# Kernel tuning notes

Measured on AMD Instinct MI355X. Metric: run time of the kernel, lower is better.

The kernel has to match this reference:

```python
import jax, jax.numpy as jnp
import numpy as np

B, Wd, C, H, F = 48, 88, 256, 32, 1024
NH_SELF, NH_CROSS = 8, 8


def _ln(x, g, b, eps=1e-5):
    mu = x.mean(-1, keepdims=True)
    var = ((x - mu) ** 2).mean(-1, keepdims=True)
    return (x - mu) / jnp.sqrt(var + eps) * g + b


def setup_inputs() -> dict:
    key = jax.random.key(0)
    ks = jax.random.split(key, 16)
    s = 0.02  # weight init scale
    d = {
        'pooled_features': jax.random.normal(ks[0], (B, Wd, C), jnp.float32),
        'features': jax.random.normal(ks[1], (B, C, H, Wd), jnp.float32),
        'self_pe': jax.random.normal(ks[2], (Wd, C), jnp.float32),
        'cross_pe': jax.random.normal(ks[3], (H, C), jnp.float32),
    }
    # LayerNorm params
    for n in ['ln_qs', 'ln_vs', 'ln_qc', 'ln_kv', 'ln_vc', 'ln_ffn']:
        d[n + '_g'] = jnp.ones((C,), jnp.float32)
        d[n + '_b'] = jnp.zeros((C,), jnp.float32)
    # attention projections (stored [in,out]; y = x @ W + b)
    names = ['Wq_s', 'Wk_s', 'Wv_s', 'Wp_s', 'Wq_c', 'Wk_c', 'Wv_c', 'Wp_c']
    for i, n in enumerate(names):
        d[n] = jax.random.normal(ks[4 + i], (C, C), jnp.float32) * s
    for n in ['bq_s', 'bv_s', 'bp_s', 'bq_c', 'bv_c', 'bp_c']:
        d[n] = jnp.zeros((C,), jnp.float32)
    # FFN
    d['W1'] = jax.random.normal(ks[12], (C, F), jnp.float32) * s
    d['b1'] = jnp.zeros((F,), jnp.float32)
    d['W2'] = jax.random.normal(ks[13], (F, C), jnp.float32) * s
    d['b2'] = jnp.zeros((C,), jnp.float32)
    return d


def reference(pooled_features, features, self_pe, cross_pe,
              ln_qs_g, ln_qs_b, ln_vs_g, ln_vs_b,
              ln_qc_g, ln_qc_b, ln_kv_g, ln_kv_b, ln_vc_g, ln_vc_b,
              ln_ffn_g, ln_ffn_b,
              Wq_s, bq_s, Wk_s, Wv_s, bv_s, Wp_s, bp_s,
              Wq_c, bq_c, Wk_c, Wv_c, bv_c, Wp_c, bp_c,
              W1, b1, W2, b2):
    b, w, c = pooled_features.shape
    h = features.shape[2]
    ds = c // NH_SELF
    dc = c // NH_CROSS

    # ---- cross attention first (op_order='cross_first', with_pe=True) ----
    xq = pooled_features                                  # [B,W,C]
    qn = _ln(xq, ln_qc_g, ln_qc_b)
    kv = jnp.transpose(features, (0, 3, 2, 1))            # [B,W,H,C]
    kn = _ln(kv + cross_pe[None, None], ln_kv_g, ln_kv_b)
    vn = _ln(kv, ln_vc_g, ln_vc_b)
    q = (qn @ Wq_c + bq_c).reshape(b, w, NH_CROSS, dc)    # query len 1 per column
    k = (kn @ Wk_c).reshape(b, w, h, NH_CROSS, dc)
    v = (vn @ Wv_c + bv_c).reshape(b, w, h, NH_CROSS, dc)
    attn = jnp.einsum('bwhd,bwkhd->bwhk', q, k) * (dc ** -0.5)
    attn = jax.nn.softmax(attn, axis=-1)
    out = jnp.einsum('bwhk,bwkhd->bwhd', attn, v).reshape(b, w, c)
    x = out @ Wp_c + bp_c + xq

    # ---- self attention over width tokens ----
    qn = _ln(x + self_pe[None], ln_qs_g, ln_qs_b)
    vn = _ln(x, ln_vs_g, ln_vs_b)
    q = (qn @ Wq_s + bq_s).reshape(b, w, NH_SELF, ds)
    k = (qn @ Wk_s).reshape(b, w, NH_SELF, ds)
    v = (vn @ Wv_s + bv_s).reshape(b, w, NH_SELF, ds)
    attn = jnp.einsum('bnhd,bmhd->bhnm', q, k) * (ds ** -0.5)
    attn = jax.nn.softmax(attn, axis=-1)
    out = jnp.einsum('bhnm,bmhd->bnhd', attn, v).reshape(b, w, c)
    x = out @ Wp_s + bp_s + x

    # ---- FFN (mmcv FFN, num_fcs=2, GELU, identity residual) ----
    hdn = _ln(x, ln_ffn_g, ln_ffn_b)
    hdn = jax.nn.gelu(hdn @ W1 + b1, approximate=False) @ W2 + b2
    return x + hdn
```

## Files before the change

### kernel.cpp

```cpp
#include <hip/hip_runtime.h>
#include <math.h>

#define B_   48
#define W_   88
#define C_   256
#define H_   32
#define F_   1024
#define BW_  (B_ * W_)
#define BWH_ (B_ * W_ * H_)
#define HW_  (H_ * W_)

typedef float  f32x4  __attribute__((ext_vector_type(4)));
typedef __bf16 bf16x8 __attribute__((ext_vector_type(8)));

__device__ __forceinline__ unsigned short f2bf(float f) {
  union { float f; unsigned int u; } v; v.f = f;
  unsigned int r = v.u + 0x7FFFu + ((v.u >> 16) & 1u);
  return (unsigned short)(r >> 16);
}
__device__ __forceinline__ float bf2f(unsigned short h) {
  union { unsigned int u; float f; } v; v.u = ((unsigned int)h) << 16;
  return v.f;
}

__global__ __launch_bounds__(256) void wt_kernel(const float* __restrict__ src,
                                                 unsigned short* __restrict__ dst,
                                                 int in_dim, int out_dim) {
  int idx = blockIdx.x * 256 + threadIdx.x;
  if (idx >= in_dim * out_dim) return;
  int i = idx % in_dim;
  int o = idx / in_dim;
  dst[idx] = f2bf(src[(size_t)i * out_dim + o]);
}

__global__ __launch_bounds__(256) void mqk_build(
    const float* __restrict__ Wq, const float* __restrict__ Wk,
    const float* __restrict__ bq,
    unsigned short* __restrict__ Mqk, float* __restrict__ bqk) {
  int n = blockIdx.x;
  int h = n >> 8, c = n & 255;
  int t = threadIdx.x;
  __shared__ float wk_s[32];
  if (t < 32) wk_s[t] = Wk[c * 256 + 32 * h + t];
  __syncthreads();
  const float scale = 0.17677669529663689f;
  float acc = 0.f;
#pragma unroll
  for (int dd = 0; dd < 32; dd++) acc += Wq[t * 256 + 32 * h + dd] * wk_s[dd];
  Mqk[(size_t)n * 256 + t] = f2bf(acc * scale);
  if (t == 0) {
    float bb = 0.f;
    for (int dd = 0; dd < 32; dd++) bb += bq[32 * h + dd] * wk_s[dd];
    bqk[n] = bb * scale;
  }
}

__global__ __launch_bounds__(256) void mvp_build(
    const float* __restrict__ Wv, const float* __restrict__ Wp,
    unsigned short* __restrict__ Mvp) {
  int d = blockIdx.x;
  int t = threadIdx.x;
  for (int h = 0; h < 8; h++) {
    float acc = 0.f;
#pragma unroll
    for (int dd = 0; dd < 32; dd++)
      acc += Wv[t * 256 + 32 * h + dd] * Wp[(32 * h + dd) * 256 + d];
    Mvp[(size_t)d * 2048 + h * 256 + t] = f2bf(acc);
  }
}

__global__ void bvp_build(const float* __restrict__ bv, const float* __restrict__ Wp,
                          const float* __restrict__ bp, float* __restrict__ bvp) {
  int d = threadIdx.x;
  float acc = bp[d];
  for (int dp = 0; dp < 256; dp++) acc += bv[dp] * Wp[dp * 256 + d];
  bvp[d] = acc;
}

__global__ __launch_bounds__(256) void ln_transpose2(
    const float* __restrict__ features, const float* __restrict__ cross_pe,
    const float* __restrict__ g_kv, const float* __restrict__ b_kv,
    const float* __restrict__ g_vc, const float* __restrict__ b_vc,
    unsigned short* __restrict__ kn, unsigned short* __restrict__ vn) {
  int b   = blockIdx.x / 88;
  int tl  = blockIdx.x % 88;
  int hw0 = tl * 32;
  __shared__ float tile[32][257];
  __shared__ float st[32][4];
  int tid = threadIdx.x;
  int l4 = (tid & 7) * 4;
  int cc = tid >> 3;
  const float* fb = features + (size_t)b * C_ * HW_ + hw0;
#pragma unroll
  for (int p = 0; p < 8; p++) {
    int c = cc + p * 32;
    float4 v = *(const float4*)(fb + (size_t)c * HW_ + l4);
    tile[l4 + 0][c] = v.x; tile[l4 + 1][c] = v.y;
    tile[l4 + 2][c] = v.z; tile[l4 + 3][c] = v.w;
  }
  __syncthreads();
  int row = tid >> 3, ln = tid & 7;
  int hr = (hw0 + row) / 88;
  const float* per = cross_pe + hr * 256;
  float s1 = 0, s2 = 0, p1 = 0, p2 = 0;
  for (int c = ln; c < 256; c += 8) {
    float v  = tile[row][c];
    float vp = v + per[c];
    s1 += v;  s2 += v * v;
    p1 += vp; p2 += vp * vp;
  }
#pragma unroll
  for (int m = 1; m < 8; m <<= 1) {
    s1 += __shfl_xor(s1, m, 8); s2 += __shfl_xor(s2, m, 8);
    p1 += __shfl_xor(p1, m, 8); p2 += __shfl_xor(p2, m, 8);
  }
  if (ln == 0) {
    float mu  = s1 * (1.f / 256.f);
    float rs  = rsqrtf(s2 * (1.f / 256.f) - mu * mu + 1e-5f);
    float muk = p1 * (1.f / 256.f);
    float rsk = rsqrtf(p2 * (1.f / 256.f) - muk * muk + 1e-5f);
    st[row][0] = mu; st[row][1] = rs; st[row][2] = muk; st[row][3] = rsk;
  }
  __syncthreads();
  int c = tid;
  float gv = g_vc[c], bv2 = b_vc[c], gk = g_kv[c], bk = b_kv[c];
  for (int r = 0; r < 32; r++) {
    int hh = (hw0 + r) / 88, ww = (hw0 + r) % 88;
    float v  = tile[r][c];
    float vp = v + cross_pe[hh * 256 + c];
    size_t ro = ((size_t)b * 88 + ww) * 32 + hh;
    vn[ro * 256 + c] = f2bf((v  - st[r][0]) * st[r][1] * gv + bv2);
    kn[ro * 256 + c] = f2bf((vp - st[r][2]) * st[r][3] * gk + bk);
  }
}

__global__ __launch_bounds__(256) void ln_rows(
    const float* __restrict__ x, const float* __restrict__ pe, int pe_mod,
    const float* __restrict__ g, const float* __restrict__ bta,
    unsigned short* __restrict__ out) {
  int row = blockIdx.x, c = threadIdx.x;
  float v = x[(size_t)row * C_ + c];
  if (pe) v += pe[(size_t)(row % pe_mod) * C_ + c];
  float s1 = v, s2 = v * v;
#pragma unroll
  for (int m = 32; m > 0; m >>= 1) {
    s1 += __shfl_xor(s1, m, 64);
    s2 += __shfl_xor(s2, m, 64);
  }
  __shared__ float red[8];
  int wave = c >> 6;
  if ((c & 63) == 0) { red[wave] = s1; red[4 + wave] = s2; }
  __syncthreads();
  s1 = red[0] + red[1] + red[2] + red[3];
  s2 = red[4] + red[5] + red[6] + red[7];
  float mu = s1 * (1.f / C_);
  float rs = rsqrtf(s2 * (1.f / C_) - mu * mu + 1e-5f);
  out[(size_t)row * C_ + c] = f2bf((v - mu) * rs * g[c] + bta[c]);
}

__global__ __launch_bounds__(256) void gemm_bt(
    const unsigned short* __restrict__ A, const unsigned short* __restrict__ Bt,
    int M, int N, int K,
    const float* __restrict__ bias, const float* __restrict__ resid,
    float* __restrict__ outF, unsigned short* __restrict__ outB, int act_gelu) {
  __shared__ __attribute__((aligned(16))) unsigned short As[64][32];
  __shared__ __attribute__((aligned(16))) unsigned short Bs[64][32];
  const int tiles_n = N >> 6;
  const int bm = blockIdx.x / tiles_n;
  const int bn = blockIdx.x % tiles_n;
  const int tid = threadIdx.x;
  const int wave = tid >> 6, lane = tid & 63;
  const int quad = lane >> 4, lr = lane & 15;
  const int wm = (wave >> 1) << 5, wn = (wave & 1) << 5;
  const int lrow = tid >> 2;
  const int lcol = (tid & 3) << 3;
  const size_t a_base = (size_t)(bm * 64 + lrow) * K + lcol;
  const size_t b_base = (size_t)(bn * 64 + lrow) * K + lcol;
  f32x4 acc[2][2] = {};
  for (int k0 = 0; k0 < K; k0 += 32) {
    *(uint4*)&As[lrow][lcol] = *(const uint4*)(A + a_base + k0);
    *(uint4*)&Bs[lrow][lcol] = *(const uint4*)(Bt + b_base + k0);
    __syncthreads();
    bf16x8 af0 = *(const bf16x8*)&As[wm + lr][quad << 3];
    bf16x8 af1 = *(const bf16x8*)&As[wm + 16 + lr][quad << 3];
    bf16x8 bf0 = *(const bf16x8*)&Bs[wn + lr][quad << 3];
    bf16x8 bf1 = *(const bf16x8*)&Bs[wn + 16 + lr][quad << 3];
    acc[0][0] = __builtin_amdgcn_mfma_f32_16x16x32_bf16(af0, bf0, acc[0][0], 0, 0, 0);
    acc[0][1] = __builtin_amdgcn_mfma_f32_16x16x32_bf16(af0, bf1, acc[0][1], 0, 0, 0);
    acc[1][0] = __builtin_amdgcn_mfma_f32_16x16x32_bf16(af1, bf0, acc[1][0], 0, 0, 0);
    acc[1][1] = __builtin_amdgcn_mfma_f32_16x16x32_bf16(af1, bf1, acc[1][1], 0, 0, 0);
    __syncthreads();
  }
#pragma unroll
  for (int i = 0; i < 2; i++)
#pragma unroll
    for (int j = 0; j < 2; j++)
#pragma unroll
      for (int rr = 0; rr < 4; rr++) {
        int row = bm * 64 + wm + i * 16 + quad * 4 + rr;
        int col = bn * 64 + wn + j * 16 + lr;
        float val = acc[i][j][rr];
        if (bias) val += bias[col];
        if (act_gelu) val = 0.5f * val * (1.f + erff(val * 0.70710678118654752f));
        if (resid) val += resid[(size_t)row * N + col];
        if (outF) outF[(size_t)row * N + col] = val;
        else outB[(size_t)row * N + col] = f2bf(val);
      }
}

#define KSTR 264
__global__ __launch_bounds__(256) void cross_attn2(
    const unsigned short* __restrict__ qt_g,
    const unsigned short* __restrict__ kn, const unsigned short* __restrict__ vn,
    unsigned short* __restrict__ ctx_g) {
  int bw = blockIdx.x;
  int tid = threadIdx.x;
  __shared__ __attribute__((aligned(16))) unsigned short qtl[8][KSTR];
  __shared__ __attribute__((aligned(16))) unsigned short knl[32][KSTR];
  __shared__ __attribute__((aligned(16))) unsigned short vnl[32][KSTR];
  __shared__ float s_sc[32 * 9];
  __shared__ float ps[8 * 36];
  __shared__ __attribute__((aligned(16))) unsigned short ctxl[2048];

  {
    uint4 qv = *(const uint4*)(qt_g + (size_t)bw * 2048 + tid * 8);
    int h = tid >> 5, c0 = (tid & 31) * 8;
    *(uint4*)&qtl[h][c0] = qv;
    int j = tid >> 3, cs = (tid & 7) * 32;
    const unsigned short* kr = kn + ((size_t)bw * 32 + j) * 256 + cs;
    const unsigned short* vr = vn + ((size_t)bw * 32 + j) * 256 + cs;
#pragma unroll
    for (int k = 0; k < 4; k++) {
      *(uint4*)&knl[j][cs + k * 8] = *(const uint4*)(kr + k * 8);
      *(uint4*)&vnl[j][cs + k * 8] = *(const uint4*)(vr + k * 8);
    }
  }
  __syncthreads();
  {
    int j = tid >> 3, h = tid & 7;
    float acc = 0.f;
#pragma unroll
    for (int c8 = 0; c8 < 32; c8++) {
      bf16x8 kk = *(const bf16x8*)&knl[j][c8 * 8];
      bf16x8 qq = *(const bf16x8*)&qtl[h][c8 * 8];
#pragma unroll
      for (int i = 0; i < 8; i++) acc += (float)qq[i] * (float)kk[i];
    }
    s_sc[j * 9 + h] = acc;
  }
  __syncthreads();
  {
    int h = tid >> 5, j = tid & 31;
    float s = s_sc[j * 9 + h];
    float mx = s;
#pragma unroll
    for (int m = 16; m > 0; m >>= 1) mx = fmaxf(mx, __shfl_xor(mx, m, 32));
    float e = __expf(s - mx);
    float sum = e;
#pragma unroll
    for (int m = 16; m > 0; m >>= 1) sum += __shfl_xor(sum, m, 32);
    ps[h * 36 + j] = e / sum;
  }
  __syncthreads();
  {
    int h = tid & 7, c0 = (tid >> 3) * 8;
    float acc[8];
#pragma unroll
    for (int i = 0; i < 8; i++) acc[i] = 0.f;
#pragma unroll 8
    for (int j = 0; j < 32; j++) {
      float p = ps[h * 36 + j];
      bf16x8 vv = *(const bf16x8*)&vnl[j][c0];
#pragma unroll
      for (int i = 0; i < 8; i++) acc[i] += p * (float)vv[i];
    }
    unsigned short pk[8];
#pragma unroll
    for (int i = 0; i < 8; i++) pk[i] = f2bf(acc[i]);
    *(uint4*)&ctxl[h * 256 + c0] = *(uint4*)pk;
  }
  __syncthreads();
  *(uint4*)(ctx_g + (size_t)bw * 2048 + tid * 8) = *(const uint4*)&ctxl[tid * 8];
}

__global__ __launch_bounds__(128) void self_attn(
    const float* __restrict__ q, const float* __restrict__ k,
    const float* __restrict__ v, unsigned short* __restrict__ out) {
  int b = blockIdx.x >> 3;
  int h = blockIdx.x & 7;
  int r = threadIdx.x;
  __shared__ float sc[W_][W_ + 1];
  if (r >= W_) return;
  size_t base = (size_t)b * W_ * C_ + h * 32;
  float qr[32];
#pragma unroll
  for (int d = 0; d < 32; d++) qr[d] = q[base + (size_t)r * C_ + d];
  for (int m = 0; m < W_; m++) {
    const float* krow = k + base + (size_t)m * C_;
    float s = 0;
#pragma unroll
    for (int d = 0; d < 32; d++) s += qr[d] * krow[d];
    sc[r][m] = s * 0.17677669529663689f;
  }
  float mx = -1e30f;
  for (int m = 0; m < W_; m++) mx = fmaxf(mx, sc[r][m]);
  float sum = 0;
  for (int m = 0; m < W_; m++) { float e = __expf(sc[r][m] - mx); sc[r][m] = e; sum += e; }
  float inv = 1.f / sum;
  float o[32];
#pragma unroll
  for (int d = 0; d < 32; d++) o[d] = 0.f;
  for (int m = 0; m < W_; m++) {
    float p = sc[r][m] * inv;
    const float* vrow = v + base + (size_t)m * C_;
#pragma unroll
    for (int d = 0; d < 32; d++) o[d] += p * vrow[d];
  }
#pragma unroll
  for (int d = 0; d < 32; d++) out[base + (size_t)r * C_ + d] = f2bf(o[d]);
}

extern "C" void kernel_launch(void* const* d_in, const int* in_sizes, int n_in,
                              void* d_out, int out_size, void* d_ws, size_t ws_size,
                              hipStream_t stream) {
  (void)in_sizes; (void)n_in; (void)out_size; (void)ws_size;
  const float* pooled   = (const float*)d_in[0];
  const float* features = (const float*)d_in[1];
  const float* self_pe  = (const float*)d_in[2];
  const float* cross_pe = (const float*)d_in[3];
  const float* ln_qs_g = (const float*)d_in[4],  *ln_qs_b = (const float*)d_in[5];
  const float* ln_vs_g = (const float*)d_in[6],  *ln_vs_b = (const float*)d_in[7];
  const float* ln_qc_g = (const float*)d_in[8],  *ln_qc_b = (const float*)d_in[9];
  const float* ln_kv_g = (const float*)d_in[10], *ln_kv_b = (const float*)d_in[11];
  const float* ln_vc_g = (const float*)d_in[12], *ln_vc_b = (const float*)d_in[13];
  const float* ln_ffn_g = (const float*)d_in[14], *ln_ffn_b = (const float*)d_in[15];
  const float* Wq_s = (const float*)d_in[16], *Wk_s = (const float*)d_in[17];
  const float* Wv_s = (const float*)d_in[18], *Wp_s = (const float*)d_in[19];
  const float* Wq_c = (const float*)d_in[20], *Wk_c = (const float*)d_in[21];
  const float* Wv_c = (const float*)d_in[22], *Wp_c = (const float*)d_in[23];
  const float* bq_s = (const float*)d_in[24], *bv_s = (const float*)d_in[25];
  const float* bp_s = (const float*)d_in[26], *bq_c = (const float*)d_in[27];
  const float* bv_c = (const float*)d_in[28], *bp_c = (const float*)d_in[29];
  const float* W1 = (const float*)d_in[30], *b1 = (const float*)d_in[31];
  const float* W2 = (const float*)d_in[32], *b2 = (const float*)d_in[33];
  float* outp = (float*)d_out;
  char* ws = (char*)d_ws;

  size_t off = 0;
  auto alloc = [&](size_t bytes) { size_t o = off; off = (off + bytes + 255) & ~(size_t)255; return o; };
  const size_t big = (size_t)BWH_ * C_ * 2;
  size_t KN  = alloc(big);
  size_t VN  = alloc(big);
  size_t QT  = alloc((size_t)BW_ * 2048 * 2);
  size_t CTX = alloc((size_t)BW_ * 2048 * 2);
  size_t MQK = alloc((size_t)2048 * 256 * 2);
  size_t MVP = alloc((size_t)256 * 2048 * 2);
  size_t BQK = alloc(2048 * 4);
  size_t BVP = alloc(256 * 4);
  size_t WQS = alloc(65536 * 2), WKS = alloc(65536 * 2);
  size_t WVS = alloc(65536 * 2), WPS = alloc(65536 * 2);
  size_t W1T = alloc(262144 * 2), W2T = alloc(262144 * 2);
  size_t QN_C = alloc((size_t)BW_ * C_ * 2);
  size_t offp = KN;
  auto allocP = [&](size_t bytes) { size_t o = offp; offp = (offp + bytes + 255) & ~(size_t)255; return o; };
  size_t X1   = allocP((size_t)BW_ * C_ * 4);
  size_t QN_S = allocP((size_t)BW_ * C_ * 2);
  size_t VN_S = allocP((size_t)BW_ * C_ * 2);
  size_t Q_S  = allocP((size_t)BW_ * C_ * 4);
  size_t K_S  = allocP((size_t)BW_ * C_ * 4);
  size_t V_S  = allocP((size_t)BW_ * C_ * 4);
  size_t S_O  = allocP((size_t)BW_ * C_ * 2);
  size_t X2   = allocP((size_t)BW_ * C_ * 4);
  size_t FFN  = allocP((size_t)BW_ * C_ * 2);
  size_t H1   = allocP((size_t)BW_ * F_ * 2);

  unsigned short* kn   = (unsigned short*)(ws + KN);
  unsigned short* vn   = (unsigned short*)(ws + VN);
  unsigned short* qt   = (unsigned short*)(ws + QT);
  unsigned short* ctx  = (unsigned short*)(ws + CTX);
  unsigned short* mqk  = (unsigned short*)(ws + MQK);
  unsigned short* mvp  = (unsigned short*)(ws + MVP);
  float* bqk = (float*)(ws + BQK);
  float* bvp = (float*)(ws + BVP);
  unsigned short* wqs = (unsigned short*)(ws + WQS), *wks = (unsigned short*)(ws + WKS);
  unsigned short* wvs = (unsigned short*)(ws + WVS), *wps = (unsigned short*)(ws + WPS);
  unsigned short* w1t = (unsigned short*)(ws + W1T), *w2t = (unsigned short*)(ws + W2T);
  unsigned short* qn_c = (unsigned short*)(ws + QN_C);
  float*          x1   = (float*)(ws + X1);
  unsigned short* qn_s = (unsigned short*)(ws + QN_S);
  unsigned short* vn_s = (unsigned short*)(ws + VN_S);
  float* q_s = (float*)(ws + Q_S), *k_s = (float*)(ws + K_S), *v_s = (float*)(ws + V_S);
  unsigned short* s_o  = (unsigned short*)(ws + S_O);
  float*          x2   = (float*)(ws + X2);
  unsigned short* ffn_n = (unsigned short*)(ws + FFN);
  unsigned short* h1    = (unsigned short*)(ws + H1);

  wt_kernel<<<256, 256, 0, stream>>>(Wq_s, wqs, 256, 256);
  wt_kernel<<<256, 256, 0, stream>>>(Wk_s, wks, 256, 256);
  wt_kernel<<<256, 256, 0, stream>>>(Wv_s, wvs, 256, 256);
  wt_kernel<<<256, 256, 0, stream>>>(Wp_s, wps, 256, 256);
  wt_kernel<<<1024, 256, 0, stream>>>(W1, w1t, 256, 1024);
  wt_kernel<<<1024, 256, 0, stream>>>(W2, w2t, 1024, 256);

  mqk_build<<<2048, 256, 0, stream>>>(Wq_c, Wk_c, bq_c, mqk, bqk);
  mvp_build<<<256, 256, 0, stream>>>(Wv_c, Wp_c, mvp);
  bvp_build<<<1, 256, 0, stream>>>(bv_c, Wp_c, bp_c, bvp);

  ln_transpose2<<<B_ * 88, 256, 0, stream>>>(features, cross_pe,
      ln_kv_g, ln_kv_b, ln_vc_g, ln_vc_b, kn, vn);

  ln_rows<<<BW_, 256, 0, stream>>>(pooled, nullptr, 1, ln_qc_g, ln_qc_b, qn_c);
  gemm_bt<<<(BW_ / 64) * (2048 / 64), 256, 0, stream>>>(qn_c, mqk, BW_, 2048, 256,
      bqk, nullptr, nullptr, qt, 0);

  cross_attn2<<<BW_, 256, 0, stream>>>(qt, kn, vn, ctx);

  gemm_bt<<<(BW_ / 64) * (C_ / 64), 256, 0, stream>>>(ctx, mvp, BW_, C_, 2048,
      bvp, pooled, x1, nullptr, 0);

  ln_rows<<<BW_, 256, 0, stream>>>(x1, self_pe, W_, ln_qs_g, ln_qs_b, qn_s);
  ln_rows<<<BW_, 256, 0, stream>>>(x1, nullptr, 1, ln_vs_g, ln_vs_b, vn_s);

  gemm_bt<<<(BW_ / 64) * (C_ / 64), 256, 0, stream>>>(qn_s, wqs, BW_, C_, C_,
      bq_s, nullptr, q_s, nullptr, 0);
  gemm_bt<<<(BW_ / 64) * (C_ / 64), 256, 0, stream>>>(qn_s, wks, BW_, C_, C_,
      nullptr, nullptr, k_s, nullptr, 0);
  gemm_bt<<<(BW_ / 64) * (C_ / 64), 256, 0, stream>>>(vn_s, wvs, BW_, C_, C_,
      bv_s, nullptr, v_s, nullptr, 0);

  self_attn<<<B_ * 8, 128, 0, stream>>>(q_s, k_s, v_s, s_o);

  gemm_bt<<<(BW_ / 64) * (C_ / 64), 256, 0, stream>>>(s_o, wps, BW_, C_, C_,
      bp_s, x1, x2, nullptr, 0);

  ln_rows<<<BW_, 256, 0, stream>>>(x2, nullptr, 1, ln_ffn_g, ln_ffn_b, ffn_n);
  gemm_bt<<<(BW_ / 64) * (F_ / 64), 256, 0, stream>>>(ffn_n, w1t, BW_, F_, C_,
      b1, nullptr, nullptr, h1, 1);
  gemm_bt<<<(BW_ / 64) * (C_ / 64), 256, 0, stream>>>(h1, w2t, BW_, C_, F_,
      b2, x2, outp, nullptr, 0);
}
```

Measured before the change: 594.0 us.

## Fuse weight prep, merge self-attn Q/K GEMM and LN, retile attention kernels

Merges the six weight-transpose launches into one kernel. Rewrites the Mqk/Mvp builders to stage weights in shared memory and run on 64 blocks instead of 2048 and 256. The cross K/V layernorm now computes statistics and writes vectorized bf16 output per thread with no second pass. The two self-attention layernorms become one kernel, and the Q and K projections become a single N=512 GEMM. Self-attention now stages K/V in shared memory and splits each head's queries across two blocks. The goals are fewer launches, better memory access and more parallel blocks, at the cost of more code and small 44-of-64-lane blocks.

```diff
diff --git a/kernel.cpp b/kernel.cpp
--- a/kernel.cpp
+++ b/kernel.cpp
@@ -22,50 +22,112 @@
   union { unsigned int u; float f; } v; v.u = ((unsigned int)h) << 16;
   return v.f;
 }
-
-__global__ __launch_bounds__(256) void wt_kernel(const float* __restrict__ src,
-                                                 unsigned short* __restrict__ dst,
-                                                 int in_dim, int out_dim) {
-  int idx = blockIdx.x * 256 + threadIdx.x;
-  if (idx >= in_dim * out_dim) return;
-  int i = idx % in_dim;
-  int o = idx / in_dim;
-  dst[idx] = f2bf(src[(size_t)i * out_dim + o]);
-}
-
-__global__ __launch_bounds__(256) void mqk_build(
+__device__ __forceinline__ unsigned int pack2(float a, float b) {
+  return (unsigned int)f2bf(a) | ((unsigned int)f2bf(b) << 16);
+}
+
+__global__ __launch_bounds__(256) void wt_all(
+    const float* __restrict__ Wq_s, const float* __restrict__ Wk_s,
+    const float* __restrict__ Wv_s, const float* __restrict__ Wp_s,
+    const float* __restrict__ W1, const float* __restrict__ W2,
+    const float* __restrict__ bq_s,
+    unsigned short* __restrict__ wqks, unsigned short* __restrict__ wvs,
+    unsigned short* __restrict__ wps, unsigned short* __restrict__ w1t,
+    unsigned short* __restrict__ w2t, float* __restrict__ bqks) {
+  int blk = blockIdx.x, t = threadIdx.x;
+  if (blk < 256) {
+    int idx = blk * 256 + t; int o = idx >> 8, i = idx & 255;
+    wqks[idx] = f2bf(Wq_s[i * 256 + o]);
+  } else if (blk < 512) {
+    int idx = (blk - 256) * 256 + t; int o = idx >> 8, i = idx & 255;
+    wqks[65536 + idx] = f2bf(Wk_s[i * 256 + o]);
+  } else if (blk < 768) {
+    int idx = (blk - 512) * 256 + t; int o = idx >> 8, i = idx & 255;
+    wvs[idx] = f2bf(Wv_s[i * 256 + o]);
+  } else if (blk < 1024) {
+    int idx = (blk - 768) * 256 + t; int o = idx >> 8, i = idx & 255;
+    wps[idx] = f2bf(Wp_s[i * 256 + o]);
+  } else if (blk < 2048) {
+    int idx = (blk - 1024) * 256 + t; int o = idx >> 8, i = idx & 255;
+    w1t[idx] = f2bf(W1[i * 1024 + o]);
+  } else if (blk < 3072) {
+    int idx = (blk - 2048) * 256 + t; int o = idx >> 10, i = idx & 1023;
+    w2t[idx] = f2bf(W2[i * 256 + o]);
+  } else {
+    bqks[t] = bq_s[t];
+    bqks[256 + t] = 0.f;
+  }
+}
+
+__global__ __launch_bounds__(256) void mqk_build2(
     const float* __restrict__ Wq, const float* __restrict__ Wk,
     const float* __restrict__ bq,
     unsigned short* __restrict__ Mqk, float* __restrict__ bqk) {
-  int n = blockIdx.x;
-  int h = n >> 8, c = n & 255;
+  int h  = blockIdx.x >> 3;
+  int cb = blockIdx.x & 7;
+  __shared__ float wq_s[256][33];
   int t = threadIdx.x;
-  __shared__ float wk_s[32];
-  if (t < 32) wk_s[t] = Wk[c * 256 + 32 * h + t];
+  int r0 = t >> 3, d4 = (t & 7) * 4;
+#pragma unroll
+  for (int j = 0; j < 8; j++) {
+    int dp = r0 + j * 32;
+    float4 v = *(const float4*)(Wq + (size_t)dp * 256 + 32 * h + d4);
+    wq_s[dp][d4 + 0] = v.x; wq_s[dp][d4 + 1] = v.y;
+    wq_s[dp][d4 + 2] = v.z; wq_s[dp][d4 + 3] = v.w;
+  }
+  int c_l = t >> 3, ln = t & 7;
+  float wk[32];
+  const float* wkr = Wk + (size_t)(32 * cb + c_l) * 256 + 32 * h;
+#pragma unroll
+  for (int j = 0; j < 8; j++) {
+    float4 v = *(const float4*)(wkr + j * 4);
+    wk[j * 4 + 0] = v.x; wk[j * 4 + 1] = v.y; wk[j * 4 + 2] = v.z; wk[j * 4 + 3] = v.w;
+  }
   __syncthreads();
   const float scale = 0.17677669529663689f;
-  float acc = 0.f;
-#pragma unroll
-  for (int dd = 0; dd < 32; dd++) acc += Wq[t * 256 + 32 * h + dd] * wk_s[dd];
-  Mqk[(size_t)n * 256 + t] = f2bf(acc * scale);
-  if (t == 0) {
+  int n = 256 * h + 32 * cb + c_l;
+  for (int i = 0; i < 32; i++) {
+    int dp = 8 * i + ln;
+    float acc = 0.f;
+#pragma unroll
+    for (int dd = 0; dd < 32; dd++) acc += wq_s[dp][dd] * wk[dd];
+    Mqk[(size_t)n * 256 + dp] = f2bf(acc * scale);
+  }
+  if (ln == 0) {
     float bb = 0.f;
-    for (int dd = 0; dd < 32; dd++) bb += bq[32 * h + dd] * wk_s[dd];
+#pragma unroll
+    for (int dd = 0; dd < 32; dd++) bb += bq[32 * h + dd] * wk[dd];
     bqk[n] = bb * scale;
   }
 }
 
-__global__ __launch_bounds__(256) void mvp_build(
+__global__ __launch_bounds__(256) void mvp_build2(
     const float* __restrict__ Wv, const float* __restrict__ Wp,
     unsigned short* __restrict__ Mvp) {
-  int d = blockIdx.x;
+  int h  = blockIdx.x >> 3;
+  int db = blockIdx.x & 7;
+  __shared__ float wv_s[256][33];
   int t = threadIdx.x;
-  for (int h = 0; h < 8; h++) {
+  int r0 = t >> 3, d4 = (t & 7) * 4;
+#pragma unroll
+  for (int j = 0; j < 8; j++) {
+    int c = r0 + j * 32;
+    float4 v = *(const float4*)(Wv + (size_t)c * 256 + 32 * h + d4);
+    wv_s[c][d4 + 0] = v.x; wv_s[c][d4 + 1] = v.y;
+    wv_s[c][d4 + 2] = v.z; wv_s[c][d4 + 3] = v.w;
+  }
+  int d_l = t >> 3, ln = t & 7;
+  int d = 32 * db + d_l;
+  float wp[32];
+#pragma unroll
+  for (int dd = 0; dd < 32; dd++) wp[dd] = Wp[(size_t)(32 * h + dd) * 256 + d];
+  __syncthreads();
+  for (int i = 0; i < 32; i++) {
+    int c = 8 * i + ln;
     float acc = 0.f;
 #pragma unroll
-    for (int dd = 0; dd < 32; dd++)
-      acc += Wv[t * 256 + 32 * h + dd] * Wp[(32 * h + dd) * 256 + d];
-    Mvp[(size_t)d * 2048 + h * 256 + t] = f2bf(acc);
+    for (int dd = 0; dd < 32; dd++) acc += wv_s[c][dd] * wp[dd];
+    Mvp[(size_t)d * 2048 + 256 * h + c] = f2bf(acc);
   }
 }
 
@@ -77,7 +139,7 @@
   bvp[d] = acc;
 }
 
-__global__ __launch_bounds__(256) void ln_transpose2(
+__global__ __launch_bounds__(256) void ln_transpose3(
     const float* __restrict__ features, const float* __restrict__ cross_pe,
     const float* __restrict__ g_kv, const float* __restrict__ b_kv,
     const float* __restrict__ g_vc, const float* __restrict__ b_vc,
@@ -85,62 +147,86 @@
   int b   = blockIdx.x / 88;
   int tl  = blockIdx.x % 88;
   int hw0 = tl * 32;
-  __shared__ float tile[32][257];
-  __shared__ float st[32][4];
+  __shared__ float tileT[256][33];
   int tid = threadIdx.x;
-  int l4 = (tid & 7) * 4;
-  int cc = tid >> 3;
-  const float* fb = features + (size_t)b * C_ * HW_ + hw0;
-#pragma unroll
-  for (int p = 0; p < 8; p++) {
-    int c = cc + p * 32;
-    float4 v = *(const float4*)(fb + (size_t)c * HW_ + l4);
-    tile[l4 + 0][c] = v.x; tile[l4 + 1][c] = v.y;
-    tile[l4 + 2][c] = v.z; tile[l4 + 3][c] = v.w;
+  {
+    int l4 = (tid & 7) * 4;
+    int cc = tid >> 3;
+    const float* fb = features + (size_t)b * C_ * HW_ + hw0;
+#pragma unroll
+    for (int p = 0; p < 8; p++) {
+      int c = cc + p * 32;
+      float4 v = *(const float4*)(fb + (size_t)c * HW_ + l4);
+      tileT[c][l4 + 0] = v.x; tileT[c][l4 + 1] = v.y;
+      tileT[c][l4 + 2] = v.z; tileT[c][l4 + 3] = v.w;
+    }
   }
   __syncthreads();
   int row = tid >> 3, ln = tid & 7;
-  int hr = (hw0 + row) / 88;
-  const float* per = cross_pe + hr * 256;
+  int hw = hw0 + row;
+  int hh = hw / 88, ww = hw - hh * 88;
+  const float* per = cross_pe + hh * 256;
+  float vreg[32], preg[32];
   float s1 = 0, s2 = 0, p1 = 0, p2 = 0;
-  for (int c = ln; c < 256; c += 8) {
-    float v  = tile[row][c];
-    float vp = v + per[c];
-    s1 += v;  s2 += v * v;
-    p1 += vp; p2 += vp * vp;
+#pragma unroll
+  for (int k = 0; k < 4; k++) {
+    int c0 = k * 64 + ln * 8;
+    float4 pa = *(const float4*)(per + c0);
+    float4 pb = *(const float4*)(per + c0 + 4);
+    float pv[8] = {pa.x, pa.y, pa.z, pa.w, pb.x, pb.y, pb.z, pb.w};
+#pragma unroll
+    for (int i = 0; i < 8; i++) {
+      float v  = tileT[c0 + i][row];
+      float vp = v + pv[i];
+      vreg[k * 8 + i] = v; preg[k * 8 + i] = pv[i];
+      s1 += v;  s2 += v * v;
+      p1 += vp; p2 += vp * vp;
+    }
   }
 #pragma unroll
   for (int m = 1; m < 8; m <<= 1) {
     s1 += __shfl_xor(s1, m, 8); s2 += __shfl_xor(s2, m, 8);
     p1 += __shfl_xor(p1, m, 8); p2 += __shfl_xor(p2, m, 8);
   }
-  if (ln == 0) {
-    float mu  = s1 * (1.f / 256.f);
-    float rs  = rsqrtf(s2 * (1.f / 256.f) - mu * mu + 1e-5f);
-    float muk = p1 * (1.f / 256.f);
-    float rsk = rsqrtf(p2 * (1.f / 256.f) - muk * muk + 1e-5f);
-    st[row][0] = mu; st[row][1] = rs; st[row][2] = muk; st[row][3] = rsk;
-  }
-  __syncthreads();
-  int c = tid;
-  float gv = g_vc[c], bv2 = b_vc[c], gk = g_kv[c], bk = b_kv[c];
-  for (int r = 0; r < 32; r++) {
-    int hh = (hw0 + r) / 88, ww = (hw0 + r) % 88;
-    float v  = tile[r][c];
-    float vp = v + cross_pe[hh * 256 + c];
-    size_t ro = ((size_t)b * 88 + ww) * 32 + hh;
-    vn[ro * 256 + c] = f2bf((v  - st[r][0]) * st[r][1] * gv + bv2);
-    kn[ro * 256 + c] = f2bf((vp - st[r][2]) * st[r][3] * gk + bk);
+  float mu  = s1 * (1.f / 256.f);
+  float rs  = rsqrtf(s2 * (1.f / 256.f) - mu * mu + 1e-5f);
+  float muk = p1 * (1.f / 256.f);
+  float rsk = rsqrtf(p2 * (1.f / 256.f) - muk * muk + 1e-5f);
+  size_t ro = ((size_t)b * 88 + ww) * 32 + hh;
+#pragma unroll
+  for (int k = 0; k < 4; k++) {
+    int c0 = k * 64 + ln * 8;
+    float gv[8], bv8[8], gk8[8], bk8[8];
+    *(float4*)&gv[0]  = *(const float4*)(g_vc + c0); *(float4*)&gv[4]  = *(const float4*)(g_vc + c0 + 4);
+    *(float4*)&bv8[0] = *(const float4*)(b_vc + c0); *(float4*)&bv8[4] = *(const float4*)(b_vc + c0 + 4);
+    *(float4*)&gk8[0] = *(const float4*)(g_kv + c0); *(float4*)&gk8[4] = *(const float4*)(g_kv + c0 + 4);
+    *(float4*)&bk8[0] = *(const float4*)(b_kv + c0); *(float4*)&bk8[4] = *(const float4*)(b_kv + c0 + 4);
+    uint4 uv, uk;
+    unsigned int pv_[4], pk_[4];
+#pragma unroll
+    for (int i = 0; i < 8; i += 2) {
+      float cg0 = gv[i] * rs, cg1 = gv[i + 1] * rs;
+      float o0 = fmaf(vreg[k * 8 + i],     cg0, fmaf(-mu, cg0, bv8[i]));
+      float o1 = fmaf(vreg[k * 8 + i + 1], cg1, fmaf(-mu, cg1, bv8[i + 1]));
+      pv_[i >> 1] = pack2(o0, o1);
+      float ck0 = gk8[i] * rsk, ck1 = gk8[i + 1] * rsk;
+      float q0 = fmaf(vreg[k * 8 + i],     ck0, fmaf(preg[k * 8 + i] - muk,     ck0, bk8[i]));
+      float q1 = fmaf(vreg[k * 8 + i + 1], ck1, fmaf(preg[k * 8 + i + 1] - muk, ck1, bk8[i + 1]));
+      pk_[i >> 1] = pack2(q0, q1);
+    }
+    uv.x = pv_[0]; uv.y = pv_[1]; uv.z = pv_[2]; uv.w = pv_[3];
+    uk.x = pk_[0]; uk.y = pk_[1]; uk.z = pk_[2]; uk.w = pk_[3];
+    *(uint4*)(vn + ro * 256 + c0) = uv;
+    *(uint4*)(kn + ro * 256 + c0) = uk;
   }
 }
 
 __global__ __launch_bounds__(256) void ln_rows(
-    const float* __restrict__ x, const float* __restrict__ pe, int pe_mod,
+    const float* __restrict__ x,
     const float* __restrict__ g, const float* __restrict__ bta,
     unsigned short* __restrict__ out) {
   int row = blockIdx.x, c = threadIdx.x;
   float v = x[(size_t)row * C_ + c];
-  if (pe) v += pe[(size_t)(row % pe_mod) * C_ + c];
   float s1 = v, s2 = v * v;
 #pragma unroll
   for (int m = 32; m > 0; m >>= 1) {
@@ -156,6 +242,36 @@
   float mu = s1 * (1.f / C_);
   float rs = rsqrtf(s2 * (1.f / C_) - mu * mu + 1e-5f);
   out[(size_t)row * C_ + c] = f2bf((v - mu) * rs * g[c] + bta[c]);
+}
+
+__global__ __launch_bounds__(256) void ln_dual(
+    const float* __restrict__ x, const float* __restrict__ pe,
+    const float* __restrict__ g1, const float* __restrict__ b1a,
+    const float* __restrict__ g2, const float* __restrict__ b2a,
+    unsigned short* __restrict__ out1, unsigned short* __restrict__ out2) {
+  int row = blockIdx.x, c = threadIdx.x;
+  float v = x[(size_t)row * C_ + c];
+  float vp = v + pe[(size_t)(row % 88) * C_ + c];
+  float s1 = v, s2 = v * v, t1 = vp, t2 = vp * vp;
+#pragma unroll
+  for (int m = 32; m > 0; m >>= 1) {
+    s1 += __shfl_xor(s1, m, 64); s2 += __shfl_xor(s2, m, 64);
+    t1 += __shfl_xor(t1, m, 64); t2 += __shfl_xor(t2, m, 64);
+  }
+  __shared__ float red[16];
+  int wave = c >> 6;
+  if ((c & 63) == 0) {
+    red[wave] = s1; red[4 + wave] = s2; red[8 + wave] = t1; red[12 + wave] = t2;
+  }
+  __syncthreads();
+  s1 = red[0] + red[1] + red[2] + red[3];
+  s2 = red[4] + red[5] + red[6] + red[7];
+  t1 = red[8] + red[9] + red[10] + red[11];
+  t2 = red[12] + red[13] + red[14] + red[15];
+  float mu = s1 * (1.f / C_), rs = rsqrtf(s2 * (1.f / C_) - mu * mu + 1e-5f);
+  float mup = t1 * (1.f / C_), rsp = rsqrtf(t2 * (1.f / C_) - mup * mup + 1e-5f);
+  out1[(size_t)row * C_ + c] = f2bf((vp - mup) * rsp * g1[c] + b1a[c]);
+  out2[(size_t)row * C_ + c] = f2bf((v - mu) * rs * g2[c] + b2a[c]);
 }
 
 __global__ __launch_bounds__(256) void gemm_bt(
@@ -221,7 +337,6 @@
   __shared__ float s_sc[32 * 9];
   __shared__ float ps[8 * 36];
   __shared__ __attribute__((aligned(16))) unsigned short ctxl[2048];
-
   {
     uint4 qv = *(const uint4*)(qt_g + (size_t)bw * 2048 + tid * 8);
     int h = tid >> 5, c0 = (tid & 31) * 8;
@@ -283,41 +398,58 @@
   *(uint4*)(ctx_g + (size_t)bw * 2048 + tid * 8) = *(const uint4*)&ctxl[tid * 8];
 }
 
-__global__ __launch_bounds__(128) void self_attn(
-    const float* __restrict__ q, const float* __restrict__ k,
-    const float* __restrict__ v, unsigned short* __restrict__ out) {
-  int b = blockIdx.x >> 3;
-  int h = blockIdx.x & 7;
-  int r = threadIdx.x;
-  __shared__ float sc[W_][W_ + 1];
-  if (r >= W_) return;
-  size_t base = (size_t)b * W_ * C_ + h * 32;
-  float qr[32];
-#pragma unroll
-  for (int d = 0; d < 32; d++) qr[d] = q[base + (size_t)r * C_ + d];
-  for (int m = 0; m < W_; m++) {
-    const float* krow = k + base + (size_t)m * C_;
-    float s = 0;
-#pragma unroll
-    for (int d = 0; d < 32; d++) s += qr[d] * krow[d];
-    sc[r][m] = s * 0.17677669529663689f;
-  }
-  float mx = -1e30f;
-  for (int m = 0; m < W_; m++) mx = fmaxf(mx, sc[r][m]);
-  float sum = 0;
-  for (int m = 0; m < W_; m++) { float e = __expf(sc[r][m] - mx); sc[r][m] = e; sum += e; }
-  float inv = 1.f / sum;
-  float o[32];
-#pragma unroll
-  for (int d = 0; d < 32; d++) o[d] = 0.f;
-  for (int m = 0; m < W_; m++) {
-    float p = sc[r][m] * inv;
-    const float* vrow = v + base + (size_t)m * C_;
-#pragma unroll
-    for (int d = 0; d < 32; d++) o[d] += p * vrow[d];
-  }
-#pragma unroll
-  for (int d = 0; d < 32; d++) out[base + (size_t)r * C_ + d] = f2bf(o[d]);
+__global__ __launch_bounds__(64) void self_attn2(
+    const float* __restrict__ qk, const float* __restrict__ v,
+    unsigned short* __restrict__ out) {
+  int blk = blockIdx.x;
+  int half = blk & 1, h = (blk >> 1) & 7, b = blk >> 4;
+  __shared__ float kl[88][32];
+  __shared__ float vl[88][32];
+  __shared__ float sc[44][89];
+  int t = threadIdx.x;
+  for (int i = t; i < 704; i += 64) {
+    int m = i >> 3, d4 = (i & 7) << 2;
+    *(float4*)&kl[m][d4] = *(const float4*)(qk + ((size_t)(b * 88 + m)) * 512 + 256 + h * 32 + d4);
+    *(float4*)&vl[m][d4] = *(const float4*)(v + ((size_t)(b * 88 + m)) * 256 + h * 32 + d4);
+  }
+  __syncthreads();
+  if (t < 44) {
+    int r = half * 44 + t;
+    const float* qrow = qk + ((size_t)(b * 88 + r)) * 512 + h * 32;
+    float qr[32];
+#pragma unroll
+    for (int d = 0; d < 32; d++) qr[d] = qrow[d];
+    float mx = -1e30f;
+    for (int m = 0; m < 88; m++) {
+      float s = 0.f;
+#pragma unroll
+      for (int d = 0; d < 32; d++) s += qr[d] * kl[m][d];
+      s *= 0.17677669529663689f;
+      sc[t][m] = s;
+      mx = fmaxf(mx, s);
+    }
+    float sum = 0.f;
+    for (int m = 0; m < 88; m++) { float e = __expf(sc[t][m] - mx); sc[t][m] = e; sum += e; }
+    float inv = 1.f / sum;
+    float o[32];
+#pragma unroll
+    for (int d = 0; d < 32; d++) o[d] = 0.f;
+    for (int m = 0; m < 88; m++) {
+      float p = sc[t][m] * inv;
+#pragma unroll
+      for (int d = 0; d < 32; d++) o[d] += p * vl[m][d];
+    }
+    unsigned short* orow = out + ((size_t)(b * 88 + r)) * 256 + h * 32;
+#pragma unroll
+    for (int g = 0; g < 4; g++) {
+      uint4 u;
+      u.x = pack2(o[g * 8 + 0], o[g * 8 + 1]);
+      u.y = pack2(o[g * 8 + 2], o[g * 8 + 3]);
+      u.z = pack2(o[g * 8 + 4], o[g * 8 + 5]);
+      u.w = pack2(o[g * 8 + 6], o[g * 8 + 7]);
+      *(uint4*)(orow + g * 8) = u;
+    }
+  }
 }
 
 extern "C" void kernel_launch(void* const* d_in, const int* in_sizes, int n_in,
@@ -357,7 +489,8 @@
   size_t MVP = alloc((size_t)256 * 2048 * 2);
   size_t BQK = alloc(2048 * 4);
   size_t BVP = alloc(256 * 4);
-  size_t WQS = alloc(65536 * 2), WKS = alloc(65536 * 2);
+  size_t WQKS = alloc((size_t)512 * 256 * 2);
+  size_t BQKS = alloc(512 * 4);
   size_t WVS = alloc(65536 * 2), WPS = alloc(65536 * 2);
   size_t W1T = alloc(262144 * 2), W2T = alloc(262144 * 2);
   size_t QN_C = alloc((size_t)BW_ * C_ * 2);
@@ -366,8 +499,7 @@
   size_t X1   = allocP((size_t)BW_ * C_ * 4);
   size_t QN_S = allocP((size_t)BW_ * C_ * 2);
   size_t VN_S = allocP((size_t)BW_ * C_ * 2);
-  size_t Q_S  = allocP((size_t)BW_ * C_ * 4);
-  size_t K_S  = allocP((size_t)BW_ * C_ * 4);
+  size_t QK_S = allocP((size_t)BW_ * 512 * 4);
   size_t V_S  = allocP((size_t)BW_ * C_ * 4);
   size_t S_O  = allocP((size_t)BW_ * C_ * 2);
   size_t X2   = allocP((size_t)BW_ * C_ * 4);
@@ -382,34 +514,31 @@
   unsigned short* mvp  = (unsigned short*)(ws + MVP);
   float* bqk = (float*)(ws + BQK);
   float* bvp = (float*)(ws + BVP);
-  unsigned short* wqs = (unsigned short*)(ws + WQS), *wks = (unsigned short*)(ws + WKS);
+  unsigned short* wqks = (unsigned short*)(ws + WQKS);
+  float* bqks = (float*)(ws + BQKS);
   unsigned short* wvs = (unsigned short*)(ws + WVS), *wps = (unsigned short*)(ws + WPS);
   unsigned short* w1t = (unsigned short*)(ws + W1T), *w2t = (unsigned short*)(ws + W2T);
   unsigned short* qn_c = (unsigned short*)(ws + QN_C);
   float*          x1   = (float*)(ws + X1);
   unsigned short* qn_s = (unsigned short*)(ws + QN_S);
   unsigned short* vn_s = (unsigned short*)(ws + VN_S);
-  float* q_s = (float*)(ws + Q_S), *k_s = (float*)(ws + K_S), *v_s = (float*)(ws + V_S);
+  float* qk_s = (float*)(ws + QK_S);
+  float* v_s  = (float*)(ws + V_S);
   unsigned short* s_o  = (unsigned short*)(ws + S_O);
   float*          x2   = (float*)(ws + X2);
   unsigned short* ffn_n = (unsigned short*)(ws + FFN);
   unsigned short* h1    = (unsigned short*)(ws + H1);
 
-  wt_kernel<<<256, 256, 0, stream>>>(Wq_s, wqs, 256, 256);
-  wt_kernel<<<256, 256, 0, stream>>>(Wk_s, wks, 256, 256);
-  wt_kernel<<<256, 256, 0, stream>>>(Wv_s, wvs, 256, 256);
-  wt_kernel<<<256, 256, 0, stream>>>(Wp_s, wps, 256, 256);
-  wt_kernel<<<1024, 256, 0, stream>>>(W1, w1t, 256, 1024);
-  wt_kernel<<<1024, 256, 0, stream>>>(W2, w2t, 1024, 256);
-
-  mqk_build<<<2048, 256, 0, stream>>>(Wq_c, Wk_c, bq_c, mqk, bqk);
-  mvp_build<<<256, 256, 0, stream>>>(Wv_c, Wp_c, mvp);
+  wt_all<<<3073, 256, 0, stream>>>(Wq_s, Wk_s, Wv_s, Wp_s, W1, W2, bq_s,
+                                   wqks, wvs, wps, w1t, w2t, bqks);
+  mqk_build2<<<64, 256, 0, stream>>>(Wq_c, Wk_c, bq_c, mqk, bqk);
+  mvp_build2<<<64, 256, 0, stream>>>(Wv_c, Wp_c, mvp);
   bvp_build<<<1, 256, 0, stream>>>(bv_c, Wp_c, bp_c, bvp);
 
-  ln_transpose2<<<B_ * 88, 256, 0, stream>>>(features, cross_pe,
+  ln_transpose3<<<B_ * 88, 256, 0, stream>>>(features, cross_pe,
       ln_kv_g, ln_kv_b, ln_vc_g, ln_vc_b, kn, vn);
 
-  ln_rows<<<BW_, 256, 0, stream>>>(pooled, nullptr, 1, ln_qc_g, ln_qc_b, qn_c);
+  ln_rows<<<BW_, 256, 0, stream>>>(pooled, ln_qc_g, ln_qc_b, qn_c);
   gemm_bt<<<(BW_ / 64) * (2048 / 64), 256, 0, stream>>>(qn_c, mqk, BW_, 2048, 256,
       bqk, nullptr, nullptr, qt, 0);
 
@@ -418,22 +547,20 @@
   gemm_bt<<<(BW_ / 64) * (C_ / 64), 256, 0, stream>>>(ctx, mvp, BW_, C_, 2048,
       bvp, pooled, x1, nullptr, 0);
 
-  ln_rows<<<BW_, 256, 0, stream>>>(x1, self_pe, W_, ln_qs_g, ln_qs_b, qn_s);
-  ln_rows<<<BW_, 256, 0, stream>>>(x1, nullptr, 1, ln_vs_g, ln_vs_b, vn_s);
-
-  gemm_bt<<<(BW_ / 64) * (C_ / 64), 256, 0, stream>>>(qn_s, wqs, BW_, C_, C_,
-      bq_s, nullptr, q_s, nullptr, 0);
-  gemm_bt<<<(BW_ / 64) * (C_ / 64), 256, 0, stream>>>(qn_s, wks, BW_, C_, C_,
-      nullptr, nullptr, k_s, nullptr, 0);
-  gemm_bt<<<(BW_ / 64) * (C_ / 64), 256, 0, stream>>>(vn_s, wvs, BW_, C_, C_,
+  ln_dual<<<BW_, 256, 0, stream>>>(x1, self_pe, ln_qs_g, ln_qs_b,
+                                   ln_vs_g, ln_vs_b, qn_s, vn_s);
+
+  gemm_bt<<<(BW_ / 64) * (512 / 64), 256, 0, stream>>>(qn_s, wqks, BW_, 512, 256,
+      bqks, nullptr, qk_s, nullptr, 0);
+  gemm_bt<<<(BW_ / 64) * (C_ / 64), 256, 0, stream>>>(vn_s, wvs, BW_, C_, 256,
       bv_s, nullptr, v_s, nullptr, 0);
 
-  self_attn<<<B_ * 8, 128, 0, stream>>>(q_s, k_s, v_s, s_o);
+  self_attn2<<<B_ * 16, 64, 0, stream>>>(qk_s, v_s, s_o);
 
   gemm_bt<<<(BW_ / 64) * (C_ / 64), 256, 0, stream>>>(s_o, wps, BW_, C_, C_,
       bp_s, x1, x2, nullptr, 0);
 
-  ln_rows<<<BW_, 256, 0, stream>>>(x2, nullptr, 1, ln_ffn_g, ln_ffn_b, ffn_n);
+  ln_rows<<<BW_, 256, 0, stream>>>(x2, ln_ffn_g, ln_ffn_b, ffn_n);
   gemm_bt<<<(BW_ / 64) * (F_ / 64), 256, 0, stream>>>(ffn_n, w1t, BW_, F_, C_,
       b1, nullptr, nullptr, h1, 1);
   gemm_bt<<<(BW_ / 64) * (C_ / 64), 256, 0, stream>>>(h1, w2t, BW_, C_, F_,
```

Result: faster. 562.6 us (-5.3%).
